# Optimization experiments

Measured on AMD Instinct MI355X. Metric: run time of the kernel, lower is better.

## Reference

```python
import jax, jax.numpy as jnp
import numpy as np

N_HEAD = 12
NEG_INF = -10000.0


def setup_inputs() -> dict:
    key = jax.random.key(0)
    k1, k2, k3 = jax.random.split(key, 3)
    B, S, D = 8, 1024, 768
    std = 0.01
    return {
        "hidden_states": jax.random.normal(k1, (B, S, D), dtype=jnp.float32),
        "Wqkv": jax.random.normal(k2, (D, 3 * D), dtype=jnp.float32) * std,
        "bqkv": jnp.zeros((3 * D,), dtype=jnp.float32),
        "Wout": jax.random.normal(k3, (D, D), dtype=jnp.float32) * std,
        "bout": jnp.zeros((D,), dtype=jnp.float32),
    }


def reference(hidden_states, Wqkv, bqkv, Wout, bout):
    B, S, D = hidden_states.shape
    H = N_HEAD
    hd = D // H
    # fused QKV projection
    qkv = hidden_states @ Wqkv + bqkv  # [B,S,3D]
    qkv = qkv.reshape(B, S, 3, H, hd)
    q, k, v = qkv[:, :, 0], qkv[:, :, 1], qkv[:, :, 2]  # [B,S,H,hd]
    q = q.transpose(0, 2, 1, 3)  # [B,H,S,hd]
    k = k.transpose(0, 2, 1, 3)
    v = v.transpose(0, 2, 1, 3)
    scale = 1.0 / jnp.sqrt(jnp.asarray(hd, dtype=hidden_states.dtype))
    scores = jnp.einsum("bhqd,bhkd->bhqk", q, k) * scale  # [B,H,S,S]
    causal = jnp.tril(jnp.ones((S, S), dtype=bool))[None, None]
    scores = jnp.where(causal, scores, jnp.asarray(NEG_INF, scores.dtype))
    probs = jax.nn.softmax(scores, axis=-1)
    # dropout is identity in eval/deterministic mode
    attn = jnp.einsum("bhqk,bhkd->bhqd", probs, v)  # [B,H,S,hd]
    attn = attn.transpose(0, 2, 1, 3).reshape(B, S, D)
    return attn @ Wout + bout
```

## Files before the change

### kernel.cpp

```cpp
#include <hip/hip_runtime.h>
#include <hip/hip_bf16.h>

#define B_   8
#define S_   1024
#define D_   768
#define H_   12
#define HD_  64
#define BS_  (B_*S_)
#define N3_  (3*D_)

typedef __attribute__((ext_vector_type(8))) short short8;
typedef __attribute__((ext_vector_type(4))) float f32x4;

__device__ __forceinline__ short8 ld8(const __hip_bfloat16* p) {
    return *reinterpret_cast<const short8*>(p);
}
__device__ __forceinline__ void st8(__hip_bfloat16* p, short8 v) {
    *reinterpret_cast<short8*>(p) = v;
}
__device__ __forceinline__ f32x4 mfma16(short8 a, short8 b, f32x4 c) {
    return __builtin_amdgcn_mfma_f32_16x16x32_bf16(a, b, c, 0, 0, 0);
}
__device__ __forceinline__ void async16(const __hip_bfloat16* g, __hip_bfloat16* l) {
    __builtin_amdgcn_global_load_lds((const __attribute__((address_space(1))) void*)g,
                                     (__attribute__((address_space(3))) void*)l,
                                     16, 0, 0);
}
__device__ __forceinline__ float fast_exp2(float x) {
#if __has_builtin(__builtin_amdgcn_exp2f)
    return __builtin_amdgcn_exp2f(x);
#else
    return __expf(x * 0.69314718056f);
#endif
}

__global__ void cast_f32_bf16(const float* __restrict__ in,
                              __hip_bfloat16* __restrict__ out, int n) {
    int i = (blockIdx.x * blockDim.x + threadIdx.x) * 4;
    if (i + 3 < n) {
        float4 v = *reinterpret_cast<const float4*>(in + i);
        out[i + 0] = __float2bfloat16(v.x);
        out[i + 1] = __float2bfloat16(v.y);
        out[i + 2] = __float2bfloat16(v.z);
        out[i + 3] = __float2bfloat16(v.w);
    }
}

__global__ void transpose_cast(const float* __restrict__ in,
                               __hip_bfloat16* __restrict__ out, int R, int C) {
    __shared__ float tile[32][33];
    int c0 = blockIdx.x * 32, r0 = blockIdx.y * 32;
    for (int i = threadIdx.y; i < 32; i += 8) {
        tile[i][threadIdx.x] = in[(size_t)(r0 + i) * C + c0 + threadIdx.x];
    }
    __syncthreads();
    for (int i = threadIdx.y; i < 32; i += 8) {
        out[(size_t)(c0 + i) * R + r0 + threadIdx.x] =
            __float2bfloat16(tile[threadIdx.x][i]);
    }
}

__global__ __launch_bounds__(256)
void gemm_qkv(const __hip_bfloat16* __restrict__ A,
              const __hip_bfloat16* __restrict__ Bt,
              const float* __restrict__ bqkv,
              __hip_bfloat16* __restrict__ Qb,
              __hip_bfloat16* __restrict__ Kb,
              __hip_bfloat16* __restrict__ Vtb) {
    __shared__ __align__(16) char smem[128 * 132 * 2];
    __hip_bfloat16* As = (__hip_bfloat16*)smem;
    __hip_bfloat16* Bs = As + 128 * 32;
    __hip_bfloat16* Ct = (__hip_bfloat16*)smem;

    int tid = threadIdx.x, wave = tid >> 6, lane = tid & 63;
    int ln = lane & 15, quad = lane >> 4;
    int mb = blockIdx.y * 128, nb = blockIdx.x * 128;
    int wm = (wave >> 1) * 64, wn = (wave & 1) * 64;

    f32x4 acc[4][4];
#pragma unroll
    for (int i = 0; i < 4; ++i)
#pragma unroll
        for (int j = 0; j < 4; ++j) acc[i][j] = (f32x4){0.f, 0.f, 0.f, 0.f};

    for (int k = 0; k < D_; k += 32) {
#pragma unroll
        for (int it = 0; it < 2; ++it) {
            int c = it * 256 + tid;
            int row = c >> 2, cc = c & 3;
            async16(A + (size_t)(mb + row) * D_ + k + cc * 8,
                    As + it * 2048 + wave * 512);
            async16(Bt + (size_t)(nb + row) * D_ + k + cc * 8,
                    Bs + it * 2048 + wave * 512);
        }
        __syncthreads();

        short8 a[4], b[4];
#pragma unroll
        for (int i = 0; i < 4; ++i)
            a[i] = ld8(As + (wm + i * 16 + ln) * 32 + quad * 8);
#pragma unroll
        for (int j = 0; j < 4; ++j)
            b[j] = ld8(Bs + (wn + j * 16 + ln) * 32 + quad * 8);
#pragma unroll
        for (int i = 0; i < 4; ++i)
#pragma unroll
            for (int j = 0; j < 4; ++j)
                acc[i][j] = mfma16(a[i], b[j], acc[i][j]);
        __syncthreads();
    }

    int which = blockIdx.x / 6;
    int nbr = nb - which * D_;
    float qscale = (which == 0) ? (0.125f * 1.44269504089f) : 1.f;

#pragma unroll
    for (int j = 0; j < 4; ++j) {
        int col = wn + j * 16 + ln;
        float bias = bqkv[nb + col];
#pragma unroll
        for (int i = 0; i < 4; ++i)
#pragma unroll
            for (int r = 0; r < 4; ++r) {
                int row = wm + i * 16 + quad * 4 + r;
                __hip_bfloat16 v = __float2bfloat16((acc[i][j][r] + bias) * qscale);
                if (which != 2) Ct[row * 132 + col] = v;
                else            Ct[col * 132 + row] = v;
            }
    }
    __syncthreads();

    int bb = mb >> 10, sb = mb & 1023;
    if (which != 2) {
        __hip_bfloat16* dst = (which == 0) ? Qb : Kb;
#pragma unroll
        for (int it = 0; it < 8; ++it) {
            int cc = it * 256 + tid;
            int row = cc >> 4, c8 = cc & 15;
            short8 v = ld8(Ct + row * 132 + c8 * 8);
            int gcol = nbr + c8 * 8;
            int h = gcol >> 6, d = gcol & 63;
            int s = sb + row;
            st8(dst + (((size_t)(bb * H_ + h)) * S_ + s) * HD_ + d, v);
        }
    } else {
#pragma unroll
        for (int it = 0; it < 8; ++it) {
            int cc = it * 256 + tid;
            int drow = cc >> 4, s8 = cc & 15;
            short8 v = ld8(Ct + drow * 132 + s8 * 8);
            int gd = nbr + drow;
            int h = gd >> 6, d = gd & 63;
            st8(Vtb + ((size_t)(bb * H_ + h) * HD_ + d) * S_ + sb + s8 * 8, v);
        }
    }
}

__global__ __launch_bounds__(256, 3)
void attn_flash3(const __hip_bfloat16* __restrict__ Q,
                 const __hip_bfloat16* __restrict__ K,
                 const __hip_bfloat16* __restrict__ Vt,
                 __hip_bfloat16* __restrict__ attnbf) {
    __shared__ __hip_bfloat16 Kbuf[2][64 * 64];
    __shared__ __hip_bfloat16 Vbuf[2][64 * 64];
    __shared__ __hip_bfloat16 Pbuf[4][32 * 72];

    int bh = blockIdx.y;
    int ip = blockIdx.x;
    int tid = threadIdx.x;
    int wave = tid >> 6, lane = tid & 63;
    int ln = lane & 15, quad = lane >> 4;
    int strip = (wave < 2) ? ip : (15 - ip);
    int qrow0 = strip * 64 + (wave & 1) * 32;

    const __hip_bfloat16* Qbh = Q + (size_t)bh * S_ * HD_;
    const __hip_bfloat16* Kbh = K + (size_t)bh * S_ * HD_;
    const __hip_bfloat16* Vbh = Vt + (size_t)bh * HD_ * S_;

    short8 aq[2][2];
#pragma unroll
    for (int rt = 0; rt < 2; ++rt)
#pragma unroll
        for (int ks = 0; ks < 2; ++ks)
            aq[rt][ks] = ld8(Qbh + (size_t)(qrow0 + rt * 16 + ln) * HD_ +
                             ks * 32 + quad * 8);

    f32x4 o[2][4];
    float l_run[2][4];
#pragma unroll
    for (int rt = 0; rt < 2; ++rt)
#pragma unroll
        for (int n = 0; n < 4; ++n) {
            o[rt][n] = (f32x4){0.f, 0.f, 0.f, 0.f};
            l_run[rt][n] = 0.f;
        }

    int last_kt = 15 - ip;

    auto stage = [&](int kt, int buf) {
        const __hip_bfloat16* gK = Kbh + (size_t)kt * 64 * HD_;
#pragma unroll
        for (int it = 0; it < 2; ++it) {
            int p = it * 256 + tid;
            int row = p >> 3;
            int csw = (p & 7) ^ (row & 7);
            async16(gK + row * HD_ + csw * 8,
                    &Kbuf[buf][it * 2048 + wave * 512]);
            async16(Vbh + (size_t)row * S_ + kt * 64 + csw * 8,
                    &Vbuf[buf][it * 2048 + wave * 512]);
        }
    };

    stage(0, 0);
    __syncthreads();
    int cur = 0;

    for (int kt = 0; kt <= last_kt; ++kt) {
        int kbase = kt * 64;
        if (kt < last_kt) stage(kt + 1, cur ^ 1);

        if (kbase <= qrow0 + 31) {
            const __hip_bfloat16* Kc = Kbuf[cur];
            const __hip_bfloat16* Vc = Vbuf[cur];

            f32x4 s[2][4];
#pragma unroll
            for (int rt = 0; rt < 2; ++rt)
#pragma unroll
                for (int j = 0; j < 4; ++j) s[rt][j] = (f32x4){0.f, 0.f, 0.f, 0.f};
#pragma unroll
            for (int j = 0; j < 4; ++j) {
                int row = j * 16 + ln;
#pragma unroll
                for (int ks = 0; ks < 2; ++ks) {
                    short8 bk = ld8(&Kc[row * 64 +
                                        (((ks * 4 + quad) ^ (row & 7)) << 3)]);
#pragma unroll
                    for (int rt = 0; rt < 2; ++rt)
                        s[rt][j] = mfma16(aq[rt][ks], bk, s[rt][j]);
                }
            }

            if (kbase + 63 > qrow0) {
#pragma unroll
                for (int rt = 0; rt < 2; ++rt)
#pragma unroll
                    for (int j = 0; j < 4; ++j) {
                        int key = kbase + j * 16 + ln;
#pragma unroll
                        for (int r = 0; r < 4; ++r) {
                            int q = qrow0 + rt * 16 + quad * 4 + r;
                            if (key > q) s[rt][j][r] = -INFINITY;
                        }
                    }
            }

#pragma unroll
            for (int rt = 0; rt < 2; ++rt)
#pragma unroll
                for (int j = 0; j < 4; ++j)
#pragma unroll
                    for (int r = 0; r < 4; ++r)
                        s[rt][j][r] = fast_exp2(s[rt][j][r]);
#pragma unroll
            for (int rt = 0; rt < 2; ++rt)
#pragma unroll
                for (int r = 0; r < 4; ++r)
                    l_run[rt][r] += (s[rt][0][r] + s[rt][1][r]) +
                                    (s[rt][2][r] + s[rt][3][r]);

#pragma unroll
            for (int rt = 0; rt < 2; ++rt)
#pragma unroll
                for (int j = 0; j < 4; ++j)
#pragma unroll
                    for (int r = 0; r < 4; ++r)
                        Pbuf[wave][(rt * 16 + quad * 4 + r) * 72 + j * 16 + ln] =
                            __float2bfloat16(s[rt][j][r]);
            asm volatile("s_waitcnt lgkmcnt(0)" ::: "memory");

            short8 ap[2][2];
#pragma unroll
            for (int rt = 0; rt < 2; ++rt)
#pragma unroll
                for (int ks = 0; ks < 2; ++ks)
                    ap[rt][ks] = ld8(&Pbuf[wave][(rt * 16 + ln) * 72 +
                                                 ks * 32 + quad * 8]);

#pragma unroll
            for (int n = 0; n < 4; ++n) {
                int row = n * 16 + ln;
#pragma unroll
                for (int ks = 0; ks < 2; ++ks) {
                    short8 bv = ld8(&Vc[row * 64 +
                                        (((ks * 4 + quad) ^ (row & 7)) << 3)]);
#pragma unroll
                    for (int rt = 0; rt < 2; ++rt)
                        o[rt][n] = mfma16(ap[rt][ks], bv, o[rt][n]);
                }
            }
        }

        __syncthreads();
        cur ^= 1;
    }

    int bb = bh / H_, h = bh - bb * H_;
#pragma unroll
    for (int rt = 0; rt < 2; ++rt)
#pragma unroll
        for (int r = 0; r < 4; ++r) {
            float l = l_run[rt][r];
            l += __shfl_xor(l, 1);
            l += __shfl_xor(l, 2);
            l += __shfl_xor(l, 4);
            l += __shfl_xor(l, 8);
            float inv = 1.f / l;
            int row = qrow0 + rt * 16 + quad * 4 + r;
#pragma unroll
            for (int n = 0; n < 4; ++n) {
                int col = h * 64 + n * 16 + ln;
                attnbf[((size_t)bb * S_ + row) * D_ + col] =
                    __float2bfloat16(o[rt][n][r] * inv);
            }
        }
}

__global__ __launch_bounds__(256)
void gemm_out(const __hip_bfloat16* __restrict__ A,
              const __hip_bfloat16* __restrict__ Bt,
              const float* __restrict__ bias,
              float* __restrict__ Cout) {
    __shared__ __align__(16) __hip_bfloat16 As[128 * 32];
    __shared__ __align__(16) __hip_bfloat16 Bs[128 * 32];

    int tid = threadIdx.x, wave = tid >> 6, lane = tid & 63;
    int ln = lane & 15, quad = lane >> 4;
    int mb = blockIdx.y * 128, nb = blockIdx.x * 128;
    int wm = (wave >> 1) * 64, wn = (wave & 1) * 64;

    f32x4 acc[4][4];
#pragma unroll
    for (int i = 0; i < 4; ++i)
#pragma unroll
        for (int j = 0; j < 4; ++j) acc[i][j] = (f32x4){0.f, 0.f, 0.f, 0.f};

    for (int k = 0; k < D_; k += 32) {
#pragma unroll
        for (int it = 0; it < 2; ++it) {
            int c = it * 256 + tid;
            int row = c >> 2, cc = c & 3;
            async16(A + (size_t)(mb + row) * D_ + k + cc * 8,
                    As + it * 2048 + wave * 512);
            async16(Bt + (size_t)(nb + row) * D_ + k + cc * 8,
                    Bs + it * 2048 + wave * 512);
        }
        __syncthreads();

        short8 a[4], b[4];
#pragma unroll
        for (int i = 0; i < 4; ++i)
            a[i] = ld8(As + (wm + i * 16 + ln) * 32 + quad * 8);
#pragma unroll
        for (int j = 0; j < 4; ++j)
            b[j] = ld8(Bs + (wn + j * 16 + ln) * 32 + quad * 8);
#pragma unroll
        for (int i = 0; i < 4; ++i)
#pragma unroll
            for (int j = 0; j < 4; ++j)
                acc[i][j] = mfma16(a[i], b[j], acc[i][j]);
        __syncthreads();
    }

#pragma unroll
    for (int j = 0; j < 4; ++j) {
        int col = nb + wn + j * 16 + ln;
        float bv = bias[col];
#pragma unroll
        for (int i = 0; i < 4; ++i)
#pragma unroll
            for (int r = 0; r < 4; ++r) {
                int row = mb + wm + i * 16 + quad * 4 + r;
                Cout[(size_t)row * D_ + col] = acc[i][j][r] + bv;
            }
    }
}

extern "C" void kernel_launch(void* const* d_in, const int* in_sizes, int n_in,
                              void* d_out, int out_size, void* d_ws, size_t ws_size,
                              hipStream_t stream) {
    const float* X    = (const float*)d_in[0];
    const float* Wqkv = (const float*)d_in[1];
    const float* bqkv = (const float*)d_in[2];
    const float* Wout = (const float*)d_in[3];
    const float* bout = (const float*)d_in[4];
    float* out = (float*)d_out;

    constexpr size_t SZ_XBF   = (size_t)BS_ * D_ * 2;
    constexpr size_t SZ_WQKVT = (size_t)N3_ * D_ * 2;
    constexpr size_t SZ_WOUTT = (size_t)D_ * D_ * 2;
    constexpr size_t SZ_QKV   = (size_t)B_ * H_ * S_ * HD_ * 2;

    char* w = (char*)d_ws;
    __hip_bfloat16* Xbf    = (__hip_bfloat16*)(w);
    __hip_bfloat16* WqkvT  = (__hip_bfloat16*)(w + SZ_XBF);
    __hip_bfloat16* WoutT  = (__hip_bfloat16*)(w + SZ_XBF + SZ_WQKVT);
    __hip_bfloat16* Qb     = (__hip_bfloat16*)(w + SZ_XBF + SZ_WQKVT + SZ_WOUTT);
    __hip_bfloat16* Kb     = (__hip_bfloat16*)(w + SZ_XBF + SZ_WQKVT + SZ_WOUTT + SZ_QKV);
    __hip_bfloat16* Vtb    = (__hip_bfloat16*)(w + SZ_XBF + SZ_WQKVT + SZ_WOUTT + 2*SZ_QKV);
    __hip_bfloat16* attnbf = (__hip_bfloat16*)(w + SZ_XBF + SZ_WQKVT + SZ_WOUTT + 3*SZ_QKV);
    (void)ws_size; (void)in_sizes; (void)n_in; (void)out_size;

    int nX = BS_ * D_;
    cast_f32_bf16<<<nX / (256 * 4), 256, 0, stream>>>(X, Xbf, nX);
    transpose_cast<<<dim3(N3_ / 32, D_ / 32), dim3(32, 8), 0, stream>>>(Wqkv, WqkvT, D_, N3_);
    transpose_cast<<<dim3(D_ / 32, D_ / 32), dim3(32, 8), 0, stream>>>(Wout, WoutT, D_, D_);

    gemm_qkv<<<dim3(N3_ / 128, BS_ / 128), 256, 0, stream>>>(Xbf, WqkvT, bqkv, Qb, Kb, Vtb);

    attn_flash3<<<dim3(8, B_ * H_), 256, 0, stream>>>(Qb, Kb, Vtb, attnbf);

    gemm_out<<<dim3(D_ / 128, BS_ / 128), 256, 0, stream>>>(attnbf, WoutT, bout, out);
}
```

Before: 197.6 us.

## Swizzle GEMM LDS tiles and split QKV epilogue into two halves

Applies an XOR swizzle to the 16-byte chunk index when staging A and B tiles into LDS in both GEMM kernels, so the MFMA fragment reads hit fewer bank conflicts. The QKV epilogue now stages the output tile in two 64-row halves, one wave pair at a time, which cuts the shared buffer from 33KB to 17KB and may raise occupancy. The cost is extra barriers and serialised epilogue writes.

```diff
diff --git a/kernel.cpp b/kernel.cpp
--- a/kernel.cpp
+++ b/kernel.cpp
@@ -67,7 +67,7 @@
               __hip_bfloat16* __restrict__ Qb,
               __hip_bfloat16* __restrict__ Kb,
               __hip_bfloat16* __restrict__ Vtb) {
-    __shared__ __align__(16) char smem[128 * 132 * 2];
+    __shared__ __align__(16) char smem[17408];
     __hip_bfloat16* As = (__hip_bfloat16*)smem;
     __hip_bfloat16* Bs = As + 128 * 32;
     __hip_bfloat16* Ct = (__hip_bfloat16*)smem;
@@ -88,20 +88,25 @@
         for (int it = 0; it < 2; ++it) {
             int c = it * 256 + tid;
             int row = c >> 2, cc = c & 3;
-            async16(A + (size_t)(mb + row) * D_ + k + cc * 8,
+            int csw = cc ^ ((row >> 1) & 3);
+            async16(A + (size_t)(mb + row) * D_ + k + csw * 8,
                     As + it * 2048 + wave * 512);
-            async16(Bt + (size_t)(nb + row) * D_ + k + cc * 8,
+            async16(Bt + (size_t)(nb + row) * D_ + k + csw * 8,
                     Bs + it * 2048 + wave * 512);
         }
         __syncthreads();
 
         short8 a[4], b[4];
 #pragma unroll
-        for (int i = 0; i < 4; ++i)
-            a[i] = ld8(As + (wm + i * 16 + ln) * 32 + quad * 8);
-#pragma unroll
-        for (int j = 0; j < 4; ++j)
-            b[j] = ld8(Bs + (wn + j * 16 + ln) * 32 + quad * 8);
+        for (int i = 0; i < 4; ++i) {
+            int row = wm + i * 16 + ln;
+            a[i] = ld8(As + row * 32 + ((quad ^ ((row >> 1) & 3)) << 3));
+        }
+#pragma unroll
+        for (int j = 0; j < 4; ++j) {
+            int row = wn + j * 16 + ln;
+            b[j] = ld8(Bs + row * 32 + ((quad ^ ((row >> 1) & 3)) << 3));
+        }
 #pragma unroll
         for (int i = 0; i < 4; ++i)
 #pragma unroll
@@ -113,46 +118,53 @@
     int which = blockIdx.x / 6;
     int nbr = nb - which * D_;
     float qscale = (which == 0) ? (0.125f * 1.44269504089f) : 1.f;
-
-#pragma unroll
-    for (int j = 0; j < 4; ++j) {
-        int col = wn + j * 16 + ln;
-        float bias = bqkv[nb + col];
-#pragma unroll
-        for (int i = 0; i < 4; ++i)
-#pragma unroll
-            for (int r = 0; r < 4; ++r) {
-                int row = wm + i * 16 + quad * 4 + r;
-                __hip_bfloat16 v = __float2bfloat16((acc[i][j][r] + bias) * qscale);
-                if (which != 2) Ct[row * 132 + col] = v;
-                else            Ct[col * 132 + row] = v;
-            }
-    }
-    __syncthreads();
-
     int bb = mb >> 10, sb = mb & 1023;
-    if (which != 2) {
-        __hip_bfloat16* dst = (which == 0) ? Qb : Kb;
-#pragma unroll
-        for (int it = 0; it < 8; ++it) {
-            int cc = it * 256 + tid;
-            int row = cc >> 4, c8 = cc & 15;
-            short8 v = ld8(Ct + row * 132 + c8 * 8);
-            int gcol = nbr + c8 * 8;
-            int h = gcol >> 6, d = gcol & 63;
-            int s = sb + row;
-            st8(dst + (((size_t)(bb * H_ + h)) * S_ + s) * HD_ + d, v);
-        }
-    } else {
-#pragma unroll
-        for (int it = 0; it < 8; ++it) {
-            int cc = it * 256 + tid;
-            int drow = cc >> 4, s8 = cc & 15;
-            short8 v = ld8(Ct + drow * 132 + s8 * 8);
-            int gd = nbr + drow;
-            int h = gd >> 6, d = gd & 63;
-            st8(Vtb + ((size_t)(bb * H_ + h) * HD_ + d) * S_ + sb + s8 * 8, v);
-        }
+
+#pragma unroll
+    for (int p = 0; p < 2; ++p) {
+        if ((wave >> 1) == p) {
+#pragma unroll
+            for (int j = 0; j < 4; ++j) {
+                int col = wn + j * 16 + ln;
+                float bias = bqkv[nb + col];
+#pragma unroll
+                for (int i = 0; i < 4; ++i)
+#pragma unroll
+                    for (int r = 0; r < 4; ++r) {
+                        int lr = i * 16 + quad * 4 + r;
+                        __hip_bfloat16 v =
+                            __float2bfloat16((acc[i][j][r] + bias) * qscale);
+                        if (which != 2) Ct[lr * 132 + col] = v;
+                        else            Ct[col * 68 + lr] = v;
+                    }
+            }
+        }
+        __syncthreads();
+        if (which != 2) {
+            __hip_bfloat16* dst = (which == 0) ? Qb : Kb;
+#pragma unroll
+            for (int it = 0; it < 4; ++it) {
+                int cc = it * 256 + tid;
+                int row = cc >> 4, c8 = cc & 15;
+                short8 v = ld8(Ct + row * 132 + c8 * 8);
+                int gcol = nbr + c8 * 8;
+                int h = gcol >> 6, d = gcol & 63;
+                int s = sb + p * 64 + row;
+                st8(dst + (((size_t)(bb * H_ + h)) * S_ + s) * HD_ + d, v);
+            }
+        } else {
+#pragma unroll
+            for (int it = 0; it < 4; ++it) {
+                int cc = it * 256 + tid;
+                int drow = cc >> 3, s8 = cc & 7;
+                short8 v = ld8(Ct + drow * 68 + s8 * 8);
+                int gd = nbr + drow;
+                int h = gd >> 6, d = gd & 63;
+                st8(Vtb + ((size_t)(bb * H_ + h) * HD_ + d) * S_ +
+                        sb + p * 64 + s8 * 8, v);
+            }
+        }
+        __syncthreads();
     }
 }
 
@@ -350,20 +362,25 @@
         for (int it = 0; it < 2; ++it) {
             int c = it * 256 + tid;
             int row = c >> 2, cc = c & 3;
-            async16(A + (size_t)(mb + row) * D_ + k + cc * 8,
+            int csw = cc ^ ((row >> 1) & 3);
+            async16(A + (size_t)(mb + row) * D_ + k + csw * 8,
                     As + it * 2048 + wave * 512);
-            async16(Bt + (size_t)(nb + row) * D_ + k + cc * 8,
+            async16(Bt + (size_t)(nb + row) * D_ + k + csw * 8,
                     Bs + it * 2048 + wave * 512);
         }
         __syncthreads();
 
         short8 a[4], b[4];
 #pragma unroll
-        for (int i = 0; i < 4; ++i)
-            a[i] = ld8(As + (wm + i * 16 + ln) * 32 + quad * 8);
-#pragma unroll
-        for (int j = 0; j < 4; ++j)
-            b[j] = ld8(Bs + (wn + j * 16 + ln) * 32 + quad * 8);
+        for (int i = 0; i < 4; ++i) {
+            int row = wm + i * 16 + ln;
+            a[i] = ld8(As + row * 32 + ((quad ^ ((row >> 1) & 3)) << 3));
+        }
+#pragma unroll
+        for (int j = 0; j < 4; ++j) {
+            int row = wn + j * 16 + ln;
+            b[j] = ld8(Bs + row * 32 + ((quad ^ ((row >> 1) & 3)) << 3));
+        }
 #pragma unroll
         for (int i = 0; i < 4; ++i)
 #pragma unroll
```

New measurement: 203.4 us. 1.03x slower.
